# Optimization experiments

Hardware: AMD Instinct MI355X
Metric: run time of the kernel (lower is better)

Reference implementation:

```python
import jax, jax.numpy as jnp
import numpy as np

BN_EPS = 1e-5


def setup_inputs() -> dict:
    key = jax.random.key(0)
    k1, k2, k3, k4 = jax.random.split(key, 4)
    N, E, D_IN, D_OUT = 100000, 1600000, 128, 128
    x = jax.random.normal(k1, (N, D_IN), dtype=jnp.float32)
    edge_index = jax.random.randint(k2, (2, E), 0, N, dtype=jnp.int64)
    # GCNConv linear (glorot) + bias (zeros init in PyG)
    W = jax.random.normal(k3, (D_OUT, D_IN), dtype=jnp.float32) * (1.0 / np.sqrt(D_IN))
    b = jnp.zeros((D_OUT,), dtype=jnp.float32)
    # BatchNorm affine params
    gamma = jnp.ones((D_OUT,), dtype=jnp.float32)
    beta = jnp.zeros((D_OUT,), dtype=jnp.float32)
    return {"x": x, "edge_index": edge_index, "W": W, "b": b,
            "gamma": gamma, "beta": beta}


def reference(x, edge_index, W, b, gamma, beta):
    N = x.shape[0]
    # --- GCNConv: add self-loops, symmetric normalization ---
    loop = jnp.arange(N, dtype=edge_index.dtype)
    src = jnp.concatenate([edge_index[0], loop])  # [E+N]
    dst = jnp.concatenate([edge_index[1], loop])  # [E+N]
    deg = jax.ops.segment_sum(jnp.ones_like(dst, dtype=x.dtype), dst,
                              num_segments=N)  # in-degree incl. self-loop
    dinv = jnp.where(deg > 0, jax.lax.rsqrt(deg), 0.0)
    norm = dinv[src] * dinv[dst]  # [E+N]
    # linear transform before propagation (PyG GCNConv)
    h = x @ W.T  # [N, D_OUT]
    agg = jax.ops.segment_sum(h[src] * norm[:, None], dst, num_segments=N)
    out = agg + b
    # --- BatchNorm1d (training mode: batch statistics over nodes) ---
    mean = jnp.mean(out, axis=0)
    var = jnp.var(out, axis=0)
    out = (out - mean) * jax.lax.rsqrt(var + BN_EPS) * gamma + beta
    # --- ReLU, residual, dropout(p=0 -> identity) ---
    out = jax.nn.relu(out)
    out = out + x  # residual (in_dim == out_dim)
    return out
```

## Files before the change

kernel.cpp:

```cpp
#include <hip/hip_runtime.h>
#include <hip/hip_fp16.h>

#define BN_EPS 1e-5f

typedef unsigned int uint32;
typedef __attribute__((ext_vector_type(8))) _Float16 f16x8;
typedef __attribute__((ext_vector_type(4))) float f32x4;

union H2U { __half2 h; uint32 u; };

__device__ __forceinline__ __half2 u2h(uint32 u) { H2U c; c.u = u; return c.h; }
__device__ __forceinline__ uint32 h2u(__half2 h) { H2U c; c.h = h; return c.u; }
__device__ __forceinline__ uint32 pack2h(float a, float b) {
    return h2u(__halves2half2(__float2half_rn(a), __float2half_rn(b)));
}
__device__ __forceinline__ float h2lo(uint32 u) {
    return __half2float(__ushort_as_half((unsigned short)(u & 0xffffu)));
}
__device__ __forceinline__ float h2hi(uint32 u) {
    return __half2float(__ushort_as_half((unsigned short)(u >> 16)));
}


__global__ void __launch_bounds__(256) k_prep_scatter(const float4* __restrict__ x4, int nx4,
                                                      const float4* __restrict__ w4, int nw4,
                                                      uint2* __restrict__ xh4, uint2* __restrict__ wh4,
                                                      const int* __restrict__ ei, int E, int NB,
                                                      int CAP, int* __restrict__ bfill,
                                                      uint32* __restrict__ bpack) {
    int t = threadIdx.x;
    if (blockIdx.x < 256) {
        __shared__ int h[4][1024];
        int wave = t >> 6;
        int c0 = (int)((long long)blockIdx.x * E / 256);
        int c1 = (int)((long long)(blockIdx.x + 1) * E / 256);
        for (int i = t; i < 4 * 1024; i += 256) h[i >> 10][i & 1023] = 0;
        __syncthreads();
        for (int e = c0 + t; e < c1; e += 256)
            atomicAdd(&h[wave][ei[E + e] >> 8], 1);
        __syncthreads();
        for (int i = t; i < NB; i += 256) {
            int n0 = h[0][i], n1 = h[1][i], n2 = h[2][i], n3 = h[3][i];
            int tot = n0 + n1 + n2 + n3;
            if (tot > 0) {
                int base = i * CAP + atomicAdd(&bfill[i], tot);
                h[0][i] = base;
                h[1][i] = base + n0;
                h[2][i] = base + n0 + n1;
                h[3][i] = base + n0 + n1 + n2;
            }
        }
        __syncthreads();
        for (int e = c0 + t; e < c1; e += 256) {
            int s = ei[e];
            int d = ei[E + e];
            int b = d >> 8;
            int pos = atomicAdd(&h[wave][b], 1);
            bpack[pos] = ((uint32)(d & 255) << 24) | (uint32)s;
        }
    } else {
        int nb = gridDim.x - 256;
        int idx = (blockIdx.x - 256) * 256 + t;
        int stride = nb * 256;
        for (int i = idx; i < nx4; i += stride) {
            float4 v = x4[i];
            xh4[i] = make_uint2(pack2h(v.x, v.y), pack2h(v.z, v.w));
        }
        for (int i = idx; i < nw4; i += stride) {
            float4 v = w4[i];
            wh4[i] = make_uint2(pack2h(v.x, v.y), pack2h(v.z, v.w));
        }
    }
}


__global__ void __launch_bounds__(256) k_csr(const uint32* __restrict__ bpack,
                                             const int* __restrict__ bfill, int CAP,
                                             int N,
                                             int* __restrict__ rowptr,
                                             int* __restrict__ rowcnt,
                                             uint32* __restrict__ dpk,
                                             int* __restrict__ col) {
    __shared__ int h[4][256], s[256], cur[4][256];
    int b = blockIdx.x;
    int t = threadIdx.x;
    int wave = t >> 6;
    int e0 = b * CAP, e1 = e0 + bfill[b];
    h[0][t] = 0; h[1][t] = 0; h[2][t] = 0; h[3][t] = 0;
    __syncthreads();
    for (int e = e0 + t; e < e1; e += 256)
        atomicAdd(&h[wave][bpack[e] >> 24], 1);
    __syncthreads();
    int n0 = h[0][t], n1 = h[1][t], n2 = h[2][t], n3 = h[3][t];
    int cnt = n0 + n1 + n2 + n3;
    s[t] = cnt;
    __syncthreads();
    for (int off = 1; off < 256; off <<= 1) {
        int add = (t >= off) ? s[t - off] : 0;
        __syncthreads();
        s[t] += add;
        __syncthreads();
    }
    int excl = s[t] - cnt;
    int node = (b << 8) + t;
    if (node < N) {
        rowptr[node] = e0 + excl;
        rowcnt[node] = cnt;
        float dv = rsqrtf((float)(cnt + 1));
        dpk[node] = pack2h(dv, dv);
    }
    cur[0][t] = e0 + excl;
    cur[1][t] = e0 + excl + n0;
    cur[2][t] = e0 + excl + n0 + n1;
    cur[3][t] = e0 + excl + n0 + n1 + n2;
    __syncthreads();
    for (int e = e0 + t; e < e1; e += 256) {
        uint32 p = bpack[e];
        int pos = atomicAdd(&cur[wave][p >> 24], 1);
        col[pos] = (int)(p & 0xffffffu);
    }
}


#define EDGE_FMA(vv, ww)                                   \
    acc0 = __hfma2(u2h((vv).x), u2h(ww), acc0);            \
    acc1 = __hfma2(u2h((vv).y), u2h(ww), acc1);            \
    acc2 = __hfma2(u2h((vv).z), u2h(ww), acc2);            \
    acc3 = __hfma2(u2h((vv).w), u2h(ww), acc3);

__global__ void __launch_bounds__(256) k_agg(const uint32* __restrict__ xh,
                                             const int* __restrict__ rowptr,
                                             const int* __restrict__ rowcnt,
                                             const int* __restrict__ col,
                                             const uint32* __restrict__ dpk,
                                             uint32* __restrict__ aggh, int N) {
    int wid = blockIdx.x * 4 + (threadIdx.x >> 6);
    if (wid >= N) return;
    int lane = threadIdx.x & 63;
    int g = lane >> 4, c = lane & 15;

    __half2 z = __float2half2_rn(0.f);
    __half2 acc0 = z, acc1 = z, acc2 = z, acc3 = z;

    int e0 = rowptr[wid];
    int e1 = e0 + rowcnt[wid];
    int e = e0;
    for (; e + 16 <= e1; e += 16) {
        int i0 = e + g, i1 = e + 4 + g, i2 = e + 8 + g, i3 = e + 12 + g;
        int s0 = col[i0], s1 = col[i1], s2 = col[i2], s3 = col[i3];
        uint32 w0 = dpk[s0], w1 = dpk[s1], w2 = dpk[s2], w3 = dpk[s3];
        uint4 v0 = *(const uint4*)&xh[(size_t)s0 * 64 + c * 4];
        uint4 v1 = *(const uint4*)&xh[(size_t)s1 * 64 + c * 4];
        uint4 v2 = *(const uint4*)&xh[(size_t)s2 * 64 + c * 4];
        uint4 v3 = *(const uint4*)&xh[(size_t)s3 * 64 + c * 4];
        EDGE_FMA(v0, w0); EDGE_FMA(v1, w1); EDGE_FMA(v2, w2); EDGE_FMA(v3, w3);
    }
    if (e < e1) {
        int i0 = e + g, i1 = e + 4 + g, i2 = e + 8 + g, i3 = e + 12 + g;
        int s0 = 0, s1 = 0, s2 = 0, s3 = 0;
        uint32 w0 = 0, w1 = 0, w2 = 0, w3 = 0;
        if (i0 < e1) { s0 = col[i0]; w0 = dpk[s0]; }
        if (i1 < e1) { s1 = col[i1]; w1 = dpk[s1]; }
        if (i2 < e1) { s2 = col[i2]; w2 = dpk[s2]; }
        if (i3 < e1) { s3 = col[i3]; w3 = dpk[s3]; }
        uint4 v0 = *(const uint4*)&xh[(size_t)s0 * 64 + c * 4];
        uint4 v1 = *(const uint4*)&xh[(size_t)s1 * 64 + c * 4];
        uint4 v2 = *(const uint4*)&xh[(size_t)s2 * 64 + c * 4];
        uint4 v3 = *(const uint4*)&xh[(size_t)s3 * 64 + c * 4];
        EDGE_FMA(v0, w0); EDGE_FMA(v1, w1); EDGE_FMA(v2, w2); EDGE_FMA(v3, w3);
    }
    uint32 u;
    u = __shfl_xor(h2u(acc0), 16); acc0 = __hadd2(acc0, u2h(u));
    u = __shfl_xor(h2u(acc0), 32); acc0 = __hadd2(acc0, u2h(u));
    u = __shfl_xor(h2u(acc1), 16); acc1 = __hadd2(acc1, u2h(u));
    u = __shfl_xor(h2u(acc1), 32); acc1 = __hadd2(acc1, u2h(u));
    u = __shfl_xor(h2u(acc2), 16); acc2 = __hadd2(acc2, u2h(u));
    u = __shfl_xor(h2u(acc2), 32); acc2 = __hadd2(acc2, u2h(u));
    u = __shfl_xor(h2u(acc3), 16); acc3 = __hadd2(acc3, u2h(u));
    u = __shfl_xor(h2u(acc3), 32); acc3 = __hadd2(acc3, u2h(u));

    if (g == 0) {
        float di = h2lo(dpk[wid]);
        uint4 sv = *(const uint4*)&xh[(size_t)wid * 64 + c * 4];
        uint4 o;
        o.x = pack2h(di * (di * h2lo(sv.x) + __low2float(acc0)),
                     di * (di * h2hi(sv.x) + __high2float(acc0)));
        o.y = pack2h(di * (di * h2lo(sv.y) + __low2float(acc1)),
                     di * (di * h2hi(sv.y) + __high2float(acc1)));
        o.z = pack2h(di * (di * h2lo(sv.z) + __low2float(acc2)),
                     di * (di * h2hi(sv.z) + __high2float(acc2)));
        o.w = pack2h(di * (di * h2lo(sv.w) + __low2float(acc3)),
                     di * (di * h2hi(sv.w) + __high2float(acc3)));
        *(uint4*)&aggh[(size_t)wid * 64 + c * 4] = o;
    }
}


#define STAGE_W()                                                            \
    for (int m = threadIdx.x; m < 2048; m += 256) {                          \
        int row = m >> 4, cc = m & 15;                                       \
        uint4 v = *(const uint4*)&Wh[row * 128 + cc * 8];                    \
        *(uint4*)((char*)wlds + row * 256 + ((cc * 16) ^ ((row & 7) << 4))) = v; \
    }

#define MFMA_TILE(acc, tile)                                                 \
    {                                                                        \
        int arow = (tile) * 64 + wave * 16 + lrow;                           \
        bool avalid = arow < N;                                              \
        _Pragma("unroll")                                                    \
        for (int kc = 0; kc < 4; ++kc) {                                     \
            f16x8 a;                                                         \
            if (avalid) a = *(const f16x8*)&Ah[(size_t)arow * 128 + kc * 32 + g * 8]; \
            else        a = (f16x8){0, 0, 0, 0, 0, 0, 0, 0};                 \
            _Pragma("unroll")                                                \
            for (int ct = 0; ct < 8; ++ct) {                                 \
                int row = ct * 16 + lrow;                                    \
                const f16x8 bfr = *(const f16x8*)((const char*)wlds + row * 256 \
                                   + ((kc * 64 + g * 16) ^ ((row & 7) << 4))); \
                acc[ct] = __builtin_amdgcn_mfma_f32_16x16x32_f16(a, bfr, acc[ct], 0, 0, 0); \
            }                                                                \
        }                                                                    \
    }

__global__ void __launch_bounds__(256) k_gemm_stats(const _Float16* __restrict__ Ah,
                                                    const _Float16* __restrict__ Wh,
                                                    const float* __restrict__ bias,
                                                    int N, int ntiles,
                                                    float* __restrict__ partials) {
    __shared__ uint32 wlds[8192];
    __shared__ float red[1024];
    STAGE_W();
    __syncthreads();

    int t = threadIdx.x;
    int wave = t >> 6, lane = t & 63;
    int lrow = lane & 15, g = lane >> 4;

    float bv[8];
    #pragma unroll
    for (int ct = 0; ct < 8; ++ct) bv[ct] = bias[ct * 16 + lrow];

    float s[8], sq[8];
    #pragma unroll
    for (int ct = 0; ct < 8; ++ct) { s[ct] = 0.f; sq[ct] = 0.f; }

    for (int tile = blockIdx.x; tile < ntiles; tile += gridDim.x) {
        f32x4 acc[8];
        #pragma unroll
        for (int ct = 0; ct < 8; ++ct) acc[ct] = (f32x4){0.f, 0.f, 0.f, 0.f};
        MFMA_TILE(acc, tile);
        int orow0 = tile * 64 + wave * 16 + g * 4;
        #pragma unroll
        for (int ct = 0; ct < 8; ++ct) {
            #pragma unroll
            for (int rr = 0; rr < 4; ++rr) {
                if (orow0 + rr < N) {
                    float o = acc[ct][rr] + bv[ct];
                    s[ct] += o; sq[ct] += o * o;
                }
            }
        }
    }
    #pragma unroll
    for (int ct = 0; ct < 8; ++ct) {
        s[ct] += __shfl_xor(s[ct], 16); sq[ct] += __shfl_xor(sq[ct], 16);
        s[ct] += __shfl_xor(s[ct], 32); sq[ct] += __shfl_xor(sq[ct], 32);
    }
    if (lane < 16) {
        #pragma unroll
        for (int ct = 0; ct < 8; ++ct) {
            int colI = ct * 16 + lrow;
            red[wave * 256 + colI] = s[ct];
            red[wave * 256 + 128 + colI] = sq[ct];
        }
    }
    __syncthreads();
    if (t < 256)
        partials[blockIdx.x * 256 + t] = red[t] + red[256 + t] + red[512 + t] + red[768 + t];
}


__global__ void __launch_bounds__(1024) k_bnparams(const float* __restrict__ partials, int nblk,
                                                   const float* __restrict__ gamma,
                                                   const float* __restrict__ beta,
                                                   float invN, float* __restrict__ ss) {
    __shared__ float red[1024];
    int tid = threadIdx.x;
    int colI = tid & 255, q = tid >> 8;
    int bq = nblk >> 2;
    float v0 = 0.f, v1 = 0.f, v2 = 0.f, v3 = 0.f;
    int b0 = q * bq;
    for (int b = b0; b < b0 + bq; b += 4) {
        v0 += partials[(b + 0) * 256 + colI];
        v1 += partials[(b + 1) * 256 + colI];
        v2 += partials[(b + 2) * 256 + colI];
        v3 += partials[(b + 3) * 256 + colI];
    }
    red[q * 256 + colI] = (v0 + v1) + (v2 + v3);
    __syncthreads();
    if (tid < 256) {
        float tot = red[tid] + red[256 + tid] + red[512 + tid] + red[768 + tid];
        red[tid] = tot;
    }
    __syncthreads();
    if (tid < 128) {
        float mean = red[tid] * invN;
        float var = red[128 + tid] * invN - mean * mean;
        float sc = gamma[tid] * rsqrtf(var + BN_EPS);
        ss[tid] = sc;
        ss[128 + tid] = beta[tid] - mean * sc;
    }
}


__global__ void __launch_bounds__(256) k_gemm_apply(const _Float16* __restrict__ Ah,
                                                    const _Float16* __restrict__ Wh,
                                                    const float* __restrict__ bias,
                                                    const float* __restrict__ ss,
                                                    const uint32* __restrict__ xh,
                                                    int N, int ntiles,
                                                    float* __restrict__ out) {
    __shared__ uint32 wlds[8192];
    STAGE_W();
    __syncthreads();

    int t = threadIdx.x;
    int wave = t >> 6, lane = t & 63;
    int lrow = lane & 15, g = lane >> 4;

    float bv[8], scv[8], shv[8];
    #pragma unroll
    for (int ct = 0; ct < 8; ++ct) {
        int colI = ct * 16 + lrow;
        bv[ct] = bias[colI]; scv[ct] = ss[colI]; shv[ct] = ss[128 + colI];
    }

    for (int tile = blockIdx.x; tile < ntiles; tile += gridDim.x) {
        f32x4 acc[8];
        #pragma unroll
        for (int ct = 0; ct < 8; ++ct) acc[ct] = (f32x4){0.f, 0.f, 0.f, 0.f};
        MFMA_TILE(acc, tile);
        int orow0 = tile * 64 + wave * 16 + g * 4;
        #pragma unroll
        for (int ct = 0; ct < 8; ++ct) {
            int ocol = ct * 16 + lrow;
            #pragma unroll
            for (int rr = 0; rr < 4; ++rr) {
                int r = orow0 + rr;
                if (r < N) {
                    float pre = acc[ct][rr] + bv[ct];
                    float o = fmaxf(pre * scv[ct] + shv[ct], 0.f);
                    uint32 xv = xh[(size_t)r * 64 + (ocol >> 1)];
                    float xr = (ocol & 1) ? h2hi(xv) : h2lo(xv);
                    out[(size_t)r * 128 + ocol] = o + xr;
                }
            }
        }
    }
}


extern "C" void kernel_launch(void* const* d_in, const int* in_sizes, int n_in,
                              void* d_out, int out_size, void* d_ws, size_t ws_size,
                              hipStream_t stream) {
    const float* x     = (const float*)d_in[0];
    const int*   ei    = (const int*)d_in[1];
    const float* W     = (const float*)d_in[2];
    const float* bias  = (const float*)d_in[3];
    const float* gamma = (const float*)d_in[4];
    const float* beta  = (const float*)d_in[5];
    float* out = (float*)d_out;

    const int D = 128;
    int N = in_sizes[0] / D;
    int E = in_sizes[1] / 2;
    int NB = (N + 255) >> 8;
    int CAP = ((E + NB - 1) / NB + 1024 + 63) & ~63;

    const int GSTATS = 256;
    const int GAPPLY = 512;

    char* ws = (char*)d_ws;
    size_t off = 0;
    auto alloc = [&](size_t bytes) -> void* {
        void* p = ws + off;
        off += (bytes + 255) & ~(size_t)255;
        return p;
    };
    uint32* xh   = (uint32*)alloc((size_t)N * 64 * sizeof(uint32));
    uint32* aggh = (uint32*)alloc((size_t)N * 64 * sizeof(uint32));
    uint32* bpack= (uint32*)alloc((size_t)NB * CAP * sizeof(uint32));
    int* col     = (int*)alloc((size_t)NB * CAP * sizeof(int));
    _Float16* Wh = (_Float16*)alloc((size_t)D * D * sizeof(_Float16));
    int* rowptr  = (int*)alloc((size_t)N * sizeof(int));
    int* rowcnt  = (int*)alloc((size_t)N * sizeof(int));
    uint32* dpk  = (uint32*)alloc((size_t)N * sizeof(uint32));
    float* ss    = (float*)alloc(256 * sizeof(float));
    float* partials = (float*)alloc((size_t)GSTATS * 256 * sizeof(float));
    int* bfill   = (int*)alloc(1024 * sizeof(int));

    hipMemsetAsync(bfill, 0, 1024 * sizeof(int), stream);

    k_prep_scatter<<<2048, 256, 0, stream>>>((const float4*)x, N * 32,
                                             (const float4*)W, D * D / 4,
                                             (uint2*)xh, (uint2*)Wh,
                                             ei, E, NB, CAP, bfill, bpack);
    k_csr<<<NB, 256, 0, stream>>>(bpack, bfill, CAP, N, rowptr, rowcnt, dpk, col);
    k_agg<<<(N + 3) / 4, 256, 0, stream>>>(xh, rowptr, rowcnt, col, dpk, aggh, N);

    int ntiles = (N + 63) / 64;
    k_gemm_stats<<<GSTATS, 256, 0, stream>>>((const _Float16*)aggh, (const _Float16*)Wh,
                                             bias, N, ntiles, partials);
    k_bnparams<<<1, 1024, 0, stream>>>(partials, GSTATS, gamma, beta, 1.0f / (float)N, ss);
    k_gemm_apply<<<GAPPLY, 256, 0, stream>>>((const _Float16*)aggh, (const _Float16*)Wh,
                                             bias, ss, xh, N, ntiles, out);
}
```

Baseline: 175.7 us.

## Fuse GEMM stats, BN params and apply into one persistent kernel with grid barrier

Merges the stats GEMM, the BN-parameter reduction and the apply GEMM into a single persistent kernel of 512 blocks. Each block holds up to four tiles of accumulators in registers, so the GEMM runs once instead of twice. A last-block-done atomic counter computes the BN scale and shift, and the other blocks spin on a flag. This removes the second pass over the aggregated features and two launches. In exchange it needs all 512 blocks co-resident, or the spin-wait deadlocks, and the larger accumulator set raises register pressure.

```diff
diff --git a/kernel.cpp b/kernel.cpp
--- a/kernel.cpp
+++ b/kernel.cpp
@@ -203,7 +203,7 @@
         *(uint4*)((char*)wlds + row * 256 + ((cc * 16) ^ ((row & 7) << 4))) = v; \
     }
 
-#define MFMA_TILE(acc, tile)                                                 \
+#define MFMA_TILE(accA, tile)                                                \
     {                                                                        \
         int arow = (tile) * 64 + wave * 16 + lrow;                           \
         bool avalid = arow < N;                                              \
@@ -217,24 +217,33 @@
                 int row = ct * 16 + lrow;                                    \
                 const f16x8 bfr = *(const f16x8*)((const char*)wlds + row * 256 \
                                    + ((kc * 64 + g * 16) ^ ((row & 7) << 4))); \
-                acc[ct] = __builtin_amdgcn_mfma_f32_16x16x32_f16(a, bfr, acc[ct], 0, 0, 0); \
+                accA[ct] = __builtin_amdgcn_mfma_f32_16x16x32_f16(a, bfr, accA[ct], 0, 0, 0); \
             }                                                                \
         }                                                                    \
     }
 
-__global__ void __launch_bounds__(256) k_gemm_stats(const _Float16* __restrict__ Ah,
-                                                    const _Float16* __restrict__ Wh,
-                                                    const float* __restrict__ bias,
-                                                    int N, int ntiles,
-                                                    float* __restrict__ partials) {
+__global__ void __launch_bounds__(256, 2) k_gemm_fused(const _Float16* __restrict__ Ah,
+                                                       const _Float16* __restrict__ Wh,
+                                                       const float* __restrict__ bias,
+                                                       const float* __restrict__ gamma,
+                                                       const float* __restrict__ beta,
+                                                       const uint32* __restrict__ xh,
+                                                       int N, int ntiles, float invN,
+                                                       float* __restrict__ partials,
+                                                       float* __restrict__ ss,
+                                                       int* __restrict__ counter,
+                                                       int* __restrict__ flag,
+                                                       float* __restrict__ out) {
     __shared__ uint32 wlds[8192];
     __shared__ float red[1024];
+    __shared__ int sh_last;
     STAGE_W();
     __syncthreads();
 
     int t = threadIdx.x;
     int wave = t >> 6, lane = t & 63;
     int lrow = lane & 15, g = lane >> 4;
+    int G = gridDim.x;
 
     float bv[8];
     #pragma unroll
@@ -244,23 +253,28 @@
     #pragma unroll
     for (int ct = 0; ct < 8; ++ct) { s[ct] = 0.f; sq[ct] = 0.f; }
 
-    for (int tile = blockIdx.x; tile < ntiles; tile += gridDim.x) {
-        f32x4 acc[8];
+    f32x4 acc[4][8];
+    #pragma unroll
+    for (int tt = 0; tt < 4; ++tt) {
         #pragma unroll
-        for (int ct = 0; ct < 8; ++ct) acc[ct] = (f32x4){0.f, 0.f, 0.f, 0.f};
-        MFMA_TILE(acc, tile);
-        int orow0 = tile * 64 + wave * 16 + g * 4;
-        #pragma unroll
-        for (int ct = 0; ct < 8; ++ct) {
+        for (int ct = 0; ct < 8; ++ct) acc[tt][ct] = (f32x4){0.f, 0.f, 0.f, 0.f};
+        int tile = blockIdx.x + tt * G;
+        if (tile < ntiles) {
+            MFMA_TILE(acc[tt], tile);
+            int orow0 = tile * 64 + wave * 16 + g * 4;
             #pragma unroll
-            for (int rr = 0; rr < 4; ++rr) {
-                if (orow0 + rr < N) {
-                    float o = acc[ct][rr] + bv[ct];
-                    s[ct] += o; sq[ct] += o * o;
+            for (int ct = 0; ct < 8; ++ct) {
+                #pragma unroll
+                for (int rr = 0; rr < 4; ++rr) {
+                    if (orow0 + rr < N) {
+                        float o = acc[tt][ct][rr] + bv[ct];
+                        s[ct] += o; sq[ct] += o * o;
+                    }
                 }
             }
         }
     }
+
     #pragma unroll
     for (int ct = 0; ct < 8; ++ct) {
         s[ct] += __shfl_xor(s[ct], 16); sq[ct] += __shfl_xor(sq[ct], 16);
@@ -277,82 +291,66 @@
     __syncthreads();
     if (t < 256)
         partials[blockIdx.x * 256 + t] = red[t] + red[256 + t] + red[512 + t] + red[768 + t];
-}
-
-
-__global__ void __launch_bounds__(1024) k_bnparams(const float* __restrict__ partials, int nblk,
-                                                   const float* __restrict__ gamma,
-                                                   const float* __restrict__ beta,
-                                                   float invN, float* __restrict__ ss) {
-    __shared__ float red[1024];
-    int tid = threadIdx.x;
-    int colI = tid & 255, q = tid >> 8;
-    int bq = nblk >> 2;
-    float v0 = 0.f, v1 = 0.f, v2 = 0.f, v3 = 0.f;
-    int b0 = q * bq;
-    for (int b = b0; b < b0 + bq; b += 4) {
-        v0 += partials[(b + 0) * 256 + colI];
-        v1 += partials[(b + 1) * 256 + colI];
-        v2 += partials[(b + 2) * 256 + colI];
-        v3 += partials[(b + 3) * 256 + colI];
-    }
-    red[q * 256 + colI] = (v0 + v1) + (v2 + v3);
-    __syncthreads();
-    if (tid < 256) {
-        float tot = red[tid] + red[256 + tid] + red[512 + tid] + red[768 + tid];
-        red[tid] = tot;
-    }
-    __syncthreads();
-    if (tid < 128) {
-        float mean = red[tid] * invN;
-        float var = red[128 + tid] * invN - mean * mean;
-        float sc = gamma[tid] * rsqrtf(var + BN_EPS);
-        ss[tid] = sc;
-        ss[128 + tid] = beta[tid] - mean * sc;
-    }
-}
-
-
-__global__ void __launch_bounds__(256) k_gemm_apply(const _Float16* __restrict__ Ah,
-                                                    const _Float16* __restrict__ Wh,
-                                                    const float* __restrict__ bias,
-                                                    const float* __restrict__ ss,
-                                                    const uint32* __restrict__ xh,
-                                                    int N, int ntiles,
-                                                    float* __restrict__ out) {
-    __shared__ uint32 wlds[8192];
-    STAGE_W();
-    __syncthreads();
-
-    int t = threadIdx.x;
-    int wave = t >> 6, lane = t & 63;
-    int lrow = lane & 15, g = lane >> 4;
-
-    float bv[8], scv[8], shv[8];
+
+    __threadfence();
+    __syncthreads();
+    if (t == 0) {
+        int prev = __hip_atomic_fetch_add(counter, 1, __ATOMIC_ACQ_REL, __HIP_MEMORY_SCOPE_AGENT);
+        sh_last = (prev == G - 1) ? 1 : 0;
+    }
+    __syncthreads();
+    if (sh_last) {
+        float v0 = 0.f, v1 = 0.f, v2 = 0.f, v3 = 0.f;
+        for (int b = 0; b < G; b += 4) {
+            v0 += partials[(b + 0) * 256 + t];
+            v1 += partials[(b + 1) * 256 + t];
+            v2 += partials[(b + 2) * 256 + t];
+            v3 += partials[(b + 3) * 256 + t];
+        }
+        red[t] = (v0 + v1) + (v2 + v3);
+        __syncthreads();
+        if (t < 128) {
+            float mean = red[t] * invN;
+            float var = red[128 + t] * invN - mean * mean;
+            float sc = gamma[t] * rsqrtf(var + BN_EPS);
+            ss[t] = sc;
+            ss[128 + t] = beta[t] - mean * sc;
+        }
+        __threadfence();
+        __syncthreads();
+        if (t == 0) __hip_atomic_store(flag, 1, __ATOMIC_RELEASE, __HIP_MEMORY_SCOPE_AGENT);
+    } else {
+        if (t == 0) {
+            while (__hip_atomic_load(flag, __ATOMIC_ACQUIRE, __HIP_MEMORY_SCOPE_AGENT) == 0)
+                __builtin_amdgcn_s_sleep(8);
+        }
+        __syncthreads();
+    }
+
+    float scv[8], shv[8];
     #pragma unroll
     for (int ct = 0; ct < 8; ++ct) {
         int colI = ct * 16 + lrow;
-        bv[ct] = bias[colI]; scv[ct] = ss[colI]; shv[ct] = ss[128 + colI];
-    }
-
-    for (int tile = blockIdx.x; tile < ntiles; tile += gridDim.x) {
-        f32x4 acc[8];
-        #pragma unroll
-        for (int ct = 0; ct < 8; ++ct) acc[ct] = (f32x4){0.f, 0.f, 0.f, 0.f};
-        MFMA_TILE(acc, tile);
-        int orow0 = tile * 64 + wave * 16 + g * 4;
-        #pragma unroll
-        for (int ct = 0; ct < 8; ++ct) {
-            int ocol = ct * 16 + lrow;
+        scv[ct] = ss[colI]; shv[ct] = ss[128 + colI];
+    }
+    #pragma unroll
+    for (int tt = 0; tt < 4; ++tt) {
+        int tile = blockIdx.x + tt * G;
+        if (tile < ntiles) {
+            int orow0 = tile * 64 + wave * 16 + g * 4;
             #pragma unroll
-            for (int rr = 0; rr < 4; ++rr) {
-                int r = orow0 + rr;
-                if (r < N) {
-                    float pre = acc[ct][rr] + bv[ct];
-                    float o = fmaxf(pre * scv[ct] + shv[ct], 0.f);
-                    uint32 xv = xh[(size_t)r * 64 + (ocol >> 1)];
-                    float xr = (ocol & 1) ? h2hi(xv) : h2lo(xv);
-                    out[(size_t)r * 128 + ocol] = o + xr;
+            for (int ct = 0; ct < 8; ++ct) {
+                int ocol = ct * 16 + lrow;
+                #pragma unroll
+                for (int rr = 0; rr < 4; ++rr) {
+                    int r = orow0 + rr;
+                    if (r < N) {
+                        float pre = acc[tt][ct][rr] + bv[ct];
+                        float o = fmaxf(pre * scv[ct] + shv[ct], 0.f);
+                        uint32 xv = xh[(size_t)r * 64 + (ocol >> 1)];
+                        float xr = (ocol & 1) ? h2hi(xv) : h2lo(xv);
+                        out[(size_t)r * 128 + ocol] = o + xr;
+                    }
                 }
             }
         }
@@ -377,8 +375,7 @@
     int NB = (N + 255) >> 8;
     int CAP = ((E + NB - 1) / NB + 1024 + 63) & ~63;
 
-    const int GSTATS = 256;
-    const int GAPPLY = 512;
+    const int GFUSED = 512;
 
     char* ws = (char*)d_ws;
     size_t off = 0;
@@ -396,10 +393,11 @@
     int* rowcnt  = (int*)alloc((size_t)N * sizeof(int));
     uint32* dpk  = (uint32*)alloc((size_t)N * sizeof(uint32));
     float* ss    = (float*)alloc(256 * sizeof(float));
-    float* partials = (float*)alloc((size_t)GSTATS * 256 * sizeof(float));
+    float* partials = (float*)alloc((size_t)GFUSED * 256 * sizeof(float));
     int* bfill   = (int*)alloc(1024 * sizeof(int));
-
-    hipMemsetAsync(bfill, 0, 1024 * sizeof(int), stream);
+    int* ctl     = (int*)alloc(64 * sizeof(int));
+
+    hipMemsetAsync(bfill, 0, 1024 * sizeof(int) + 64 * sizeof(int), stream);
 
     k_prep_scatter<<<2048, 256, 0, stream>>>((const float4*)x, N * 32,
                                              (const float4*)W, D * D / 4,
@@ -409,9 +407,8 @@
     k_agg<<<(N + 3) / 4, 256, 0, stream>>>(xh, rowptr, rowcnt, col, dpk, aggh, N);
 
     int ntiles = (N + 63) / 64;
-    k_gemm_stats<<<GSTATS, 256, 0, stream>>>((const _Float16*)aggh, (const _Float16*)Wh,
-                                             bias, N, ntiles, partials);
-    k_bnparams<<<1, 1024, 0, stream>>>(partials, GSTATS, gamma, beta, 1.0f / (float)N, ss);
-    k_gemm_apply<<<GAPPLY, 256, 0, stream>>>((const _Float16*)aggh, (const _Float16*)Wh,
-                                             bias, ss, xh, N, ntiles, out);
-}
+    k_gemm_fused<<<GFUSED, 256, 0, stream>>>((const _Float16*)aggh, (const _Float16*)Wh,
+                                             bias, gamma, beta, xh,
+                                             N, ntiles, 1.0f / (float)N,
+                                             partials, ss, &ctl[0], &ctl[1], out);
+}
```

After: 410.2 us. 134% more time.
